# Kernel tuning notes

Hardware: AMD Instinct MI355X
Metric: run time of the kernel (lower is better)

The kernel has to match this reference:

```python
import jax, jax.numpy as jnp
import numpy as np

D = 448  # state_dim == input_dim == output_dim

def _param(key, shape):
    # matches torch.rand(shape) * 0.1 + 0.001
    return jax.random.uniform(key, shape, dtype=jnp.float32) * 0.1 + 0.001

def setup_inputs() -> dict:
    key = jax.random.key(0)
    ks = jax.random.split(key, 9)
    x = jax.random.normal(ks[0], (8, 4096, D), dtype=jnp.float32)
    return {
        "x": x,
        "W_q": _param(ks[1], (D, D)),
        "W_k": _param(ks[2], (D, D)),
        "W_v": _param(ks[3], (D, D)),
        "W_o": _param(ks[4], (D, D)),
        "SSM_A": _param(ks[5], (D, D)),
        "SSM_B": _param(ks[6], (D, D)),
        "SSM_C": _param(ks[7], (D, D)),
    }

def reference(x, W_q, W_k, W_v, W_o, SSM_A, SSM_B, SSM_C):
    # seq_len=4096 > threshold=256 -> quadratic SSM path.
    # structured_processing's einsum 'bsd,dd->bsd' multiplies elementwise by
    # the diagonal of the matrix; the block loop is redundant, so we apply the
    # diagonal scale over the whole sequence in one fused op.
    q = jnp.einsum('bsi,id->bsd', x, W_q)
    k = jnp.einsum('bsi,id->bsd', x, W_k)
    v = jnp.einsum('bsi,id->bsd', x, W_v)
    ssm = (q * jnp.diagonal(SSM_A)
           + k * jnp.diagonal(SSM_B)
           + v * jnp.diagonal(SSM_C))
    # dropout is identity in eval mode
    return jnp.einsum('bsd,do->bso', ssm, W_o)
```

## Files before the change

kernel.cpp:

```cpp
#include <hip/hip_runtime.h>
#include <hip/hip_bf16.h>

#define DDIM 448

typedef __hip_bfloat16 bf16;
typedef __attribute__((ext_vector_type(8))) short short8;
typedef __attribute__((ext_vector_type(4))) float f32x4;

__device__ __forceinline__ short bf_bits(float f) {
    bf16 h = __float2bfloat16(f);
    return *reinterpret_cast<short*>(&h);
}

__device__ __forceinline__ void async16(const bf16* g, bf16* l) {
    __builtin_amdgcn_global_load_lds(
        (const __attribute__((address_space(1))) void*)g,
        (__attribute__((address_space(3))) void*)l, 16, 0, 0);
}

__global__ __launch_bounds__(256) void prep_wc(
    const float* __restrict__ Wq, const float* __restrict__ Wk,
    const float* __restrict__ Wv, const float* __restrict__ Wo,
    const float* __restrict__ Ad, const float* __restrict__ Bd,
    const float* __restrict__ Cd, bf16* __restrict__ WcT)
{
    __shared__ __align__(16) bf16 As[64 * 32];
    __shared__ __align__(16) bf16 Bs[64 * 32];
    __shared__ float da[DDIM], db[DDIM], dc[DDIM];

    const int tid  = threadIdx.x;
    const int i0   = blockIdx.x * 64;
    const int o0   = blockIdx.y * 64;
    const int lane = tid & 63;
    const int wid  = tid >> 6;
    const int wm   = wid >> 1, wn = wid & 1;
    const int m_   = lane & 15, kq = lane >> 4;

    for (int d = tid; d < DDIM; d += 256) {
        da[d] = Ad[d * DDIM + d];
        db[d] = Bd[d * DDIM + d];
        dc[d] = Cd[d * DDIM + d];
    }

    const int dr  = tid >> 3;
    const int oc8 = (tid & 7) * 8;
    const int ir  = tid >> 2;
    const int dc8 = (tid & 3) * 8;

    f32x4 acc[2][2] = {};

    f32x4 w0 = *(const f32x4*)(Wo + dr * DDIM + o0 + oc8);
    f32x4 w1 = *(const f32x4*)(Wo + dr * DDIM + o0 + oc8 + 4);
    f32x4 q0 = *(const f32x4*)(Wq + (i0 + ir) * DDIM + dc8);
    f32x4 q1 = *(const f32x4*)(Wq + (i0 + ir) * DDIM + dc8 + 4);
    f32x4 t0 = *(const f32x4*)(Wk + (i0 + ir) * DDIM + dc8);
    f32x4 t1 = *(const f32x4*)(Wk + (i0 + ir) * DDIM + dc8 + 4);
    f32x4 v0 = *(const f32x4*)(Wv + (i0 + ir) * DDIM + dc8);
    f32x4 v1 = *(const f32x4*)(Wv + (i0 + ir) * DDIM + dc8 + 4);

    for (int k0 = 0; k0 < DDIM; k0 += 32) {
        __syncthreads();

        #pragma unroll
        for (int j = 0; j < 4; ++j) {
            As[(oc8 + j) * 32 + dr]     = __float2bfloat16(w0[j]);
            As[(oc8 + 4 + j) * 32 + dr] = __float2bfloat16(w1[j]);
        }
        short8 e;
        #pragma unroll
        for (int j = 0; j < 4; ++j) {
            e[j]     = bf_bits(q0[j] * da[k0 + dc8 + j]
                             + t0[j] * db[k0 + dc8 + j]
                             + v0[j] * dc[k0 + dc8 + j]);
            e[j + 4] = bf_bits(q1[j] * da[k0 + dc8 + 4 + j]
                             + t1[j] * db[k0 + dc8 + 4 + j]
                             + v1[j] * dc[k0 + dc8 + 4 + j]);
        }
        *(short8*)&Bs[ir * 32 + dc8] = e;
        __syncthreads();

        const int kn = (k0 + 32 < DDIM) ? k0 + 32 : 0;
        w0 = *(const f32x4*)(Wo + (kn + dr) * DDIM + o0 + oc8);
        w1 = *(const f32x4*)(Wo + (kn + dr) * DDIM + o0 + oc8 + 4);
        q0 = *(const f32x4*)(Wq + (i0 + ir) * DDIM + kn + dc8);
        q1 = *(const f32x4*)(Wq + (i0 + ir) * DDIM + kn + dc8 + 4);
        t0 = *(const f32x4*)(Wk + (i0 + ir) * DDIM + kn + dc8);
        t1 = *(const f32x4*)(Wk + (i0 + ir) * DDIM + kn + dc8 + 4);
        v0 = *(const f32x4*)(Wv + (i0 + ir) * DDIM + kn + dc8);
        v1 = *(const f32x4*)(Wv + (i0 + ir) * DDIM + kn + dc8 + 4);

        short8 af[2], bfr[2];
        #pragma unroll
        for (int mi = 0; mi < 2; ++mi)
            af[mi] = *(const short8*)&As[(wm * 32 + mi * 16 + m_) * 32 + kq * 8];
        #pragma unroll
        for (int ni = 0; ni < 2; ++ni)
            bfr[ni] = *(const short8*)&Bs[(wn * 32 + ni * 16 + m_) * 32 + kq * 8];
        #pragma unroll
        for (int mi = 0; mi < 2; ++mi)
            #pragma unroll
            for (int ni = 0; ni < 2; ++ni)
                acc[mi][ni] = __builtin_amdgcn_mfma_f32_16x16x32_bf16(
                    af[mi], bfr[ni], acc[mi][ni], 0, 0, 0);
    }

    #pragma unroll
    for (int mi = 0; mi < 2; ++mi)
        #pragma unroll
        for (int ni = 0; ni < 2; ++ni) {
            const int o = o0 + wm * 32 + mi * 16 + kq * 4;
            const int i = i0 + wn * 32 + ni * 16 + m_;
            #pragma unroll
            for (int r = 0; r < 4; ++r)
                WcT[(o + r) * DDIM + i] = __float2bfloat16(acc[mi][ni][r]);
        }
}

__global__ __launch_bounds__(256, 2) void gemm_xwc(
    const float* __restrict__ X, const bf16* __restrict__ WcT,
    float* __restrict__ out)
{
    __shared__ __align__(16) char smem[61440];
    bf16* As  = (bf16*)smem;
    bf16* Bs0 = (bf16*)(smem + 4096);
    bf16* Bs1 = (bf16*)(smem + 32768);
    float* Cb = (float*)(smem + 4096);

    const int tid  = threadIdx.x;
    const int lane = tid & 63;
    const int wid  = tid >> 6;
    const int m_   = lane & 15;
    const int kq   = lane >> 4;
    const int row0 = blockIdx.x * 64;

    const int ar = tid >> 2;
    const int ac = (tid & 3) * 8;
    const float* agp = X + (row0 + ar) * DDIM + ac;

    const int lrow = lane >> 2;
    const int lcol = (lane & 3) * 8;

    f32x4 acc[4][7] = {};

    #pragma unroll
    for (int j = 0; j < 7; ++j)
        async16(WcT + ((wid * 7 + j) * 16 + lrow) * DDIM + lcol,
                Bs0 + (wid * 7 + j) * 16 * 32);
    f32x4 a0 = *(const f32x4*)agp;
    f32x4 a1 = *(const f32x4*)(agp + 4);

    int s = 0;
    for (int k0 = 0; k0 < DDIM; k0 += 32, ++s) {
        __syncthreads();
        short8 w;
        #pragma unroll
        for (int j = 0; j < 4; ++j) {
            w[j]     = bf_bits(a0[j]);
            w[j + 4] = bf_bits(a1[j]);
        }
        *(short8*)&As[ar * 32 + ac] = w;
        __syncthreads();

        const int kn = k0 + 32;
        if (kn < DDIM) {
            bf16* Bnxt = ((s + 1) & 1) ? Bs1 : Bs0;
            #pragma unroll
            for (int j = 0; j < 7; ++j)
                async16(WcT + ((wid * 7 + j) * 16 + lrow) * DDIM + kn + lcol,
                        Bnxt + (wid * 7 + j) * 16 * 32);
            a0 = *(const f32x4*)(agp + kn);
            a1 = *(const f32x4*)(agp + kn + 4);
        }

        const bf16* Bcur = (s & 1) ? Bs1 : Bs0;
        short8 af[4], bfr[7];
        #pragma unroll
        for (int mi = 0; mi < 4; ++mi)
            af[mi] = *(const short8*)&As[(mi * 16 + m_) * 32 + kq * 8];
        #pragma unroll
        for (int ni = 0; ni < 7; ++ni)
            bfr[ni] = *(const short8*)&Bcur[(wid * 112 + ni * 16 + m_) * 32 + kq * 8];

        #pragma unroll
        for (int mi = 0; mi < 4; ++mi)
            #pragma unroll
            for (int ni = 0; ni < 7; ++ni)
                acc[mi][ni] = __builtin_amdgcn_mfma_f32_16x16x32_bf16(
                    af[mi], bfr[ni], acc[mi][ni], 0, 0, 0);
    }

    #pragma unroll
    for (int mi = 0; mi < 4; ++mi) {
        __syncthreads();
        #pragma unroll
        for (int ni = 0; ni < 7; ++ni) {
            const int col = wid * 112 + ni * 16 + m_;
            #pragma unroll
            for (int r = 0; r < 4; ++r)
                Cb[(kq * 4 + r) * DDIM + col] = acc[mi][ni][r];
        }
        __syncthreads();
        float* dst = out + (row0 + mi * 16) * DDIM;
        #pragma unroll
        for (int j = 0; j < 7; ++j)
            ((f32x4*)dst)[j * 256 + tid] = ((const f32x4*)Cb)[j * 256 + tid];
    }
}

extern "C" void kernel_launch(void* const* d_in, const int* in_sizes, int n_in,
                              void* d_out, int out_size, void* d_ws, size_t ws_size,
                              hipStream_t stream) {
    const float* x  = (const float*)d_in[0];
    const float* Wq = (const float*)d_in[1];
    const float* Wk = (const float*)d_in[2];
    const float* Wv = (const float*)d_in[3];
    const float* Wo = (const float*)d_in[4];
    const float* Ad = (const float*)d_in[5];
    const float* Bd = (const float*)d_in[6];
    const float* Cd = (const float*)d_in[7];

    bf16*  WcT = (bf16*)d_ws;
    float* out = (float*)d_out;

    const int M = in_sizes[0] / DDIM;

    prep_wc<<<dim3(7, 7), 256, 0, stream>>>(Wq, Wk, Wv, Wo, Ad, Bd, Cd, WcT);
    gemm_xwc<<<M / 64, 256, 0, stream>>>(x, WcT, out);
}
```

Before: 156.3 us.

## Double M tile to 128 rows and double-buffer A tile with one barrier per step

```diff
diff --git a/kernel.cpp b/kernel.cpp
--- a/kernel.cpp
+++ b/kernel.cpp
@@ -2,6 +2,7 @@
 #include <hip/hip_bf16.h>
 
 #define DDIM 448
+#define NSTEP 14
 
 typedef __hip_bfloat16 bf16;
 typedef __attribute__((ext_vector_type(8))) short short8;
@@ -60,7 +61,6 @@
 
     for (int k0 = 0; k0 < DDIM; k0 += 32) {
         __syncthreads();
-
         #pragma unroll
         for (int j = 0; j < 4; ++j) {
             As[(oc8 + j) * 32 + dr]     = __float2bfloat16(w0[j]);
@@ -116,94 +116,124 @@
         }
 }
 
-__global__ __launch_bounds__(256, 2) void gemm_xwc(
+__global__ __launch_bounds__(256, 1) void gemm_xwc(
     const float* __restrict__ X, const bf16* __restrict__ WcT,
     float* __restrict__ out)
 {
-    __shared__ __align__(16) char smem[61440];
-    bf16* As  = (bf16*)smem;
-    bf16* Bs0 = (bf16*)(smem + 4096);
-    bf16* Bs1 = (bf16*)(smem + 32768);
-    float* Cb = (float*)(smem + 4096);
+    __shared__ __align__(16) char smem[73728];
 
     const int tid  = threadIdx.x;
     const int lane = tid & 63;
     const int wid  = tid >> 6;
     const int m_   = lane & 15;
     const int kq   = lane >> 4;
-    const int row0 = blockIdx.x * 64;
-
-    const int ar = tid >> 2;
-    const int ac = (tid & 3) * 8;
+    const int row0 = blockIdx.x * 128;
+
+    const int ar = tid >> 1;
+    const int ac = (tid & 1) * 16;
     const float* agp = X + (row0 + ar) * DDIM + ac;
 
     const int lrow = lane >> 2;
     const int lcol = (lane & 3) * 8;
-
-    f32x4 acc[4][7] = {};
-
-    #pragma unroll
-    for (int j = 0; j < 7; ++j)
-        async16(WcT + ((wid * 7 + j) * 16 + lrow) * DDIM + lcol,
-                Bs0 + (wid * 7 + j) * 16 * 32);
-    f32x4 a0 = *(const f32x4*)agp;
+    const bf16* bgp = WcT + (wid * 112 + lrow) * DDIM + lcol;
+
+    f32x4 acc[8][7] = {};
+
+    {
+        bf16* B0 = (bf16*)(smem + 16384);
+        #pragma unroll
+        for (int j = 0; j < 7; ++j)
+            async16(bgp + j * 16 * DDIM, B0 + (wid * 7 + j) * 16 * 32);
+    }
+
+    f32x4 a0 = *(const f32x4*)(agp);
     f32x4 a1 = *(const f32x4*)(agp + 4);
-
-    int s = 0;
-    for (int k0 = 0; k0 < DDIM; k0 += 32, ++s) {
-        __syncthreads();
-        short8 w;
+    f32x4 a2 = *(const f32x4*)(agp + 8);
+    f32x4 a3 = *(const f32x4*)(agp + 12);
+    {
+        bf16* A0 = (bf16*)smem;
+        short8 w0, w1;
         #pragma unroll
         for (int j = 0; j < 4; ++j) {
-            w[j]     = bf_bits(a0[j]);
-            w[j + 4] = bf_bits(a1[j]);
-        }
-        *(short8*)&As[ar * 32 + ac] = w;
-        __syncthreads();
-
-        const int kn = k0 + 32;
-        if (kn < DDIM) {
-            bf16* Bnxt = ((s + 1) & 1) ? Bs1 : Bs0;
+            w0[j] = bf_bits(a0[j]); w0[j + 4] = bf_bits(a1[j]);
+            w1[j] = bf_bits(a2[j]); w1[j + 4] = bf_bits(a3[j]);
+        }
+        *(short8*)&A0[ar * 32 + ac]     = w0;
+        *(short8*)&A0[ar * 32 + ac + 8] = w1;
+    }
+    a0 = *(const f32x4*)(agp + 32);
+    a1 = *(const f32x4*)(agp + 36);
+    a2 = *(const f32x4*)(agp + 40);
+    a3 = *(const f32x4*)(agp + 44);
+    __syncthreads();
+
+    for (int s = 0; s < NSTEP; ++s) {
+        const int cur = s & 1, nxt = cur ^ 1;
+        const bf16* Ac = (const bf16*)(smem + (cur << 13));
+        const bf16* Bc = (const bf16*)(smem + 16384 + cur * 28672);
+
+        if (s + 1 < NSTEP) {
+            bf16* An = (bf16*)(smem + (nxt << 13));
+            bf16* Bn = (bf16*)(smem + 16384 + nxt * 28672);
+            short8 w0, w1;
+            #pragma unroll
+            for (int j = 0; j < 4; ++j) {
+                w0[j] = bf_bits(a0[j]); w0[j + 4] = bf_bits(a1[j]);
+                w1[j] = bf_bits(a2[j]); w1[j + 4] = bf_bits(a3[j]);
+            }
+            *(short8*)&An[ar * 32 + ac]     = w0;
+            *(short8*)&An[ar * 32 + ac + 8] = w1;
+            const int kn = (s + 1) * 32;
             #pragma unroll
             for (int j = 0; j < 7; ++j)
-                async16(WcT + ((wid * 7 + j) * 16 + lrow) * DDIM + kn + lcol,
-                        Bnxt + (wid * 7 + j) * 16 * 32);
-            a0 = *(const f32x4*)(agp + kn);
-            a1 = *(const f32x4*)(agp + kn + 4);
-        }
-
-        const bf16* Bcur = (s & 1) ? Bs1 : Bs0;
-        short8 af[4], bfr[7];
-        #pragma unroll
-        for (int mi = 0; mi < 4; ++mi)
-            af[mi] = *(const short8*)&As[(mi * 16 + m_) * 32 + kq * 8];
+                async16(bgp + j * 16 * DDIM + kn, Bn + (wid * 7 + j) * 16 * 32);
+            if (s + 2 < NSTEP) {
+                const int k2 = (s + 2) * 32;
+                a0 = *(const f32x4*)(agp + k2);
+                a1 = *(const f32x4*)(agp + k2 + 4);
+                a2 = *(const f32x4*)(agp + k2 + 8);
+                a3 = *(const f32x4*)(agp + k2 + 12);
+            }
+        }
+
+        short8 af[8], bfr[7];
+        #pragma unroll
+        for (int mi = 0; mi < 8; ++mi)
+            af[mi] = *(const short8*)&Ac[(mi * 16 + m_) * 32 + kq * 8];
         #pragma unroll
         for (int ni = 0; ni < 7; ++ni)
-            bfr[ni] = *(const short8*)&Bcur[(wid * 112 + ni * 16 + m_) * 32 + kq * 8];
-
-        #pragma unroll
-        for (int mi = 0; mi < 4; ++mi)
+            bfr[ni] = *(const short8*)&Bc[(wid * 112 + ni * 16 + m_) * 32 + kq * 8];
+
+        #pragma unroll
+        for (int mi = 0; mi < 8; ++mi)
             #pragma unroll
             for (int ni = 0; ni < 7; ++ni)
                 acc[mi][ni] = __builtin_amdgcn_mfma_f32_16x16x32_bf16(
                     af[mi], bfr[ni], acc[mi][ni], 0, 0, 0);
-    }
-
+
+        __syncthreads();
+    }
+
+    float* Cb = (float*)(smem + 16384);
     #pragma unroll
-    for (int mi = 0; mi < 4; ++mi) {
-        __syncthreads();
-        #pragma unroll
-        for (int ni = 0; ni < 7; ++ni) {
-            const int col = wid * 112 + ni * 16 + m_;
-            #pragma unroll
-            for (int r = 0; r < 4; ++r)
-                Cb[(kq * 4 + r) * DDIM + col] = acc[mi][ni][r];
-        }
-        __syncthreads();
-        float* dst = out + (row0 + mi * 16) * DDIM;
-        #pragma unroll
-        for (int j = 0; j < 7; ++j)
+    for (int t = 0; t < 4; ++t) {
+        #pragma unroll
+        for (int mi2 = 0; mi2 < 2; ++mi2) {
+            const int mi = t * 2 + mi2;
+            #pragma unroll
+            for (int ni = 0; ni < 7; ++ni) {
+                const int col = wid * 112 + ni * 16 + m_;
+                #pragma unroll
+                for (int r = 0; r < 4; ++r)
+                    Cb[(mi2 * 16 + kq * 4 + r) * DDIM + col] = acc[mi][ni][r];
+            }
+        }
+        __syncthreads();
+        float* dst = out + (row0 + t * 32) * DDIM;
+        #pragma unroll
+        for (int j = 0; j < 14; ++j)
             ((f32x4*)dst)[j * 256 + tid] = ((const f32x4*)Cb)[j * 256 + tid];
+        __syncthreads();
     }
 }
 
@@ -225,5 +255,5 @@
     const int M = in_sizes[0] / DDIM;
 
     prep_wc<<<dim3(7, 7), 256, 0, stream>>>(Wq, Wk, Wv, Wo, Ad, Bd, Cd, WcT);
-    gemm_xwc<<<M / 64, 256, 0, stream>>>(x, WcT, out);
-}
+    gemm_xwc<<<M / 128, 256, 0, stream>>>(x, WcT, out);
+}
```

After: 147.6 us. 1.06x faster.

## Stage full X tile in LDS and stream WcT fragments from global into registers

Applied to the files above, without the earlier changes.

```diff
diff --git a/kernel.cpp b/kernel.cpp
--- a/kernel.cpp
+++ b/kernel.cpp
@@ -2,6 +2,8 @@
 #include <hip/hip_bf16.h>
 
 #define DDIM 448
+#define NSTEP 14
+#define ASTRIDE 456
 
 typedef __hip_bfloat16 bf16;
 typedef __attribute__((ext_vector_type(8))) short short8;
@@ -10,12 +12,6 @@
 __device__ __forceinline__ short bf_bits(float f) {
     bf16 h = __float2bfloat16(f);
     return *reinterpret_cast<short*>(&h);
-}
-
-__device__ __forceinline__ void async16(const bf16* g, bf16* l) {
-    __builtin_amdgcn_global_load_lds(
-        (const __attribute__((address_space(1))) void*)g,
-        (__attribute__((address_space(3))) void*)l, 16, 0, 0);
 }
 
 __global__ __launch_bounds__(256) void prep_wc(
@@ -60,7 +56,6 @@
 
     for (int k0 = 0; k0 < DDIM; k0 += 32) {
         __syncthreads();
-
         #pragma unroll
         for (int j = 0; j < 4; ++j) {
             As[(oc8 + j) * 32 + dr]     = __float2bfloat16(w0[j]);
@@ -116,94 +111,109 @@
         }
 }
 
-__global__ __launch_bounds__(256, 2) void gemm_xwc(
+__global__ __launch_bounds__(512, 2) void gemm_xwc(
     const float* __restrict__ X, const bf16* __restrict__ WcT,
     float* __restrict__ out)
 {
-    __shared__ __align__(16) char smem[61440];
-    bf16* As  = (bf16*)smem;
-    bf16* Bs0 = (bf16*)(smem + 4096);
-    bf16* Bs1 = (bf16*)(smem + 32768);
-    float* Cb = (float*)(smem + 4096);
+    __shared__ __align__(16) char smem[128 * ASTRIDE * 2];
+    bf16* As = (bf16*)smem;
 
     const int tid  = threadIdx.x;
     const int lane = tid & 63;
-    const int wid  = tid >> 6;
+    const int wv   = tid >> 6;
+    const int wm   = wv >> 2;
+    const int wn   = wv & 3;
     const int m_   = lane & 15;
     const int kq   = lane >> 4;
-    const int row0 = blockIdx.x * 64;
-
-    const int ar = tid >> 2;
-    const int ac = (tid & 3) * 8;
-    const float* agp = X + (row0 + ar) * DDIM + ac;
-
-    const int lrow = lane >> 2;
-    const int lcol = (lane & 3) * 8;
+    const int row0 = blockIdx.x * 128;
+
+    {
+        const int ar  = tid >> 2;
+        const int ac  = (tid & 3) * 8;
+        const float* agp = X + (row0 + ar) * DDIM + ac;
+        #pragma unroll
+        for (int ko = 0; ko < NSTEP; ++ko) {
+            f32x4 x0 = *(const f32x4*)(agp + ko * 32);
+            f32x4 x1 = *(const f32x4*)(agp + ko * 32 + 4);
+            short8 w;
+            #pragma unroll
+            for (int j = 0; j < 4; ++j) {
+                w[j]     = bf_bits(x0[j]);
+                w[j + 4] = bf_bits(x1[j]);
+            }
+            *(short8*)&As[ar * ASTRIDE + ko * 32 + ac] = w;
+        }
+    }
+    __syncthreads();
+
+    const bf16* bgp = WcT + (wn * 112 + m_) * DDIM + kq * 8;
+    const int arow = wm * 64;
 
     f32x4 acc[4][7] = {};
-
+    short8 b0[7], b1[7];
     #pragma unroll
-    for (int j = 0; j < 7; ++j)
-        async16(WcT + ((wid * 7 + j) * 16 + lrow) * DDIM + lcol,
-                Bs0 + (wid * 7 + j) * 16 * 32);
-    f32x4 a0 = *(const f32x4*)agp;
-    f32x4 a1 = *(const f32x4*)(agp + 4);
-
-    int s = 0;
-    for (int k0 = 0; k0 < DDIM; k0 += 32, ++s) {
-        __syncthreads();
-        short8 w;
-        #pragma unroll
-        for (int j = 0; j < 4; ++j) {
-            w[j]     = bf_bits(a0[j]);
-            w[j + 4] = bf_bits(a1[j]);
-        }
-        *(short8*)&As[ar * 32 + ac] = w;
-        __syncthreads();
-
-        const int kn = k0 + 32;
-        if (kn < DDIM) {
-            bf16* Bnxt = ((s + 1) & 1) ? Bs1 : Bs0;
-            #pragma unroll
-            for (int j = 0; j < 7; ++j)
-                async16(WcT + ((wid * 7 + j) * 16 + lrow) * DDIM + kn + lcol,
-                        Bnxt + (wid * 7 + j) * 16 * 32);
-            a0 = *(const f32x4*)(agp + kn);
-            a1 = *(const f32x4*)(agp + kn + 4);
-        }
-
-        const bf16* Bcur = (s & 1) ? Bs1 : Bs0;
-        short8 af[4], bfr[7];
-        #pragma unroll
-        for (int mi = 0; mi < 4; ++mi)
-            af[mi] = *(const short8*)&As[(mi * 16 + m_) * 32 + kq * 8];
+    for (int ni = 0; ni < 7; ++ni)
+        b0[ni] = *(const short8*)(bgp + ni * 16 * DDIM);
+
+    for (int s = 0; s < NSTEP; s += 2) {
         #pragma unroll
         for (int ni = 0; ni < 7; ++ni)
-            bfr[ni] = *(const short8*)&Bcur[(wid * 112 + ni * 16 + m_) * 32 + kq * 8];
-
-        #pragma unroll
-        for (int mi = 0; mi < 4; ++mi)
+            b1[ni] = *(const short8*)(bgp + ni * 16 * DDIM + (s + 1) * 32);
+        {
+            short8 af[4];
+            #pragma unroll
+            for (int mi = 0; mi < 4; ++mi)
+                af[mi] = *(const short8*)&As[(arow + mi * 16 + m_) * ASTRIDE
+                                             + s * 32 + kq * 8];
+            #pragma unroll
+            for (int mi = 0; mi < 4; ++mi)
+                #pragma unroll
+                for (int ni = 0; ni < 7; ++ni)
+                    acc[mi][ni] = __builtin_amdgcn_mfma_f32_16x16x32_bf16(
+                        af[mi], b0[ni], acc[mi][ni], 0, 0, 0);
+        }
+        if (s + 2 < NSTEP) {
             #pragma unroll
             for (int ni = 0; ni < 7; ++ni)
-                acc[mi][ni] = __builtin_amdgcn_mfma_f32_16x16x32_bf16(
-                    af[mi], bfr[ni], acc[mi][ni], 0, 0, 0);
-    }
-
+                b0[ni] = *(const short8*)(bgp + ni * 16 * DDIM + (s + 2) * 32);
+        }
+        {
+            short8 af[4];
+            #pragma unroll
+            for (int mi = 0; mi < 4; ++mi)
+                af[mi] = *(const short8*)&As[(arow + mi * 16 + m_) * ASTRIDE
+                                             + (s + 1) * 32 + kq * 8];
+            #pragma unroll
+            for (int mi = 0; mi < 4; ++mi)
+                #pragma unroll
+                for (int ni = 0; ni < 7; ++ni)
+                    acc[mi][ni] = __builtin_amdgcn_mfma_f32_16x16x32_bf16(
+                        af[mi], b1[ni], acc[mi][ni], 0, 0, 0);
+        }
+    }
+
+    float* Cb = (float*)smem;
     #pragma unroll
-    for (int mi = 0; mi < 4; ++mi) {
-        __syncthreads();
-        #pragma unroll
-        for (int ni = 0; ni < 7; ++ni) {
-            const int col = wid * 112 + ni * 16 + m_;
-            #pragma unroll
-            for (int r = 0; r < 4; ++r)
-                Cb[(kq * 4 + r) * DDIM + col] = acc[mi][ni][r];
-        }
-        __syncthreads();
-        float* dst = out + (row0 + mi * 16) * DDIM;
+    for (int t = 0; t < 4; ++t) {
+        __syncthreads();
+        if (wm == (t >> 1)) {
+            #pragma unroll
+            for (int p = 0; p < 2; ++p) {
+                const int mi = (t & 1) * 2 + p;
+                #pragma unroll
+                for (int ni = 0; ni < 7; ++ni) {
+                    const int col = wn * 112 + ni * 16 + m_;
+                    #pragma unroll
+                    for (int r = 0; r < 4; ++r)
+                        Cb[(p * 16 + kq * 4 + r) * DDIM + col] = acc[mi][ni][r];
+                }
+            }
+        }
+        __syncthreads();
+        float* dst = out + (row0 + t * 32) * DDIM;
         #pragma unroll
         for (int j = 0; j < 7; ++j)
-            ((f32x4*)dst)[j * 256 + tid] = ((const f32x4*)Cb)[j * 256 + tid];
+            ((f32x4*)dst)[j * 512 + tid] = ((const f32x4*)Cb)[j * 512 + tid];
     }
 }
 
@@ -225,5 +235,5 @@
     const int M = in_sizes[0] / DDIM;
 
     prep_wc<<<dim3(7, 7), 256, 0, stream>>>(Wq, Wk, Wv, Wo, Ad, Bd, Cd, WcT);
-    gemm_xwc<<<M / 64, 256, 0, stream>>>(x, WcT, out);
-}
+    gemm_xwc<<<M / 128, 512, 0, stream>>>(x, WcT, out);
+}
```

New measurement: 152.3 us. 1.03x faster.
